# Kernel tuning notes

Measured on AMD Instinct MI355X. Metric: run time of the kernel, lower is better.

## Reference

```python
import jax, jax.numpy as jnp
import numpy as np

N, E, G = 50000, 800000, 64
IN, HID, T, EDGE_DIM, HLS = 32, 64, 2, 2, 32
# deg histogram: all nodes degree 16 -> avg_deg['log'] = log(16+1)
AVG_LOG = float(np.log(17.0))


def _pna(x, src, dst, eattr, We, be, Wpre, bpre, Wpost, bpost, Wlin, blin):
    """PNAConv with aggregators [mean,min,max,std], scalers [identity,amp,att],
    towers=T, pre_layers=1, post_layers=1, divide_input=False."""
    n, F = x.shape
    enc = eattr @ We + be                                   # [E, F] edge encoder
    # message: concat(x_i, x_j, edge) -> per-tower Linear(3F -> F)
    h = jnp.concatenate([x[dst], x[src], enc], axis=-1)     # [E, 3F] (same for all towers)
    m = jnp.einsum('ef,tfo->eto', h, Wpre) + bpre           # [E, T, F]
    ones = jnp.ones((m.shape[0],), m.dtype)
    cnt = jax.ops.segment_sum(ones, dst, num_segments=n)    # in-degree [N]
    d = jnp.maximum(cnt, 1.0)[:, None, None]
    s = jax.ops.segment_sum(m, dst, num_segments=n)
    mean = s / d
    msq = jax.ops.segment_sum(m * m, dst, num_segments=n) / d
    std = jnp.sqrt(jax.nn.relu(msq - mean * mean) + 1e-5)
    has = (cnt > 0)[:, None, None]
    mn = jnp.where(has, jax.ops.segment_min(m, dst, num_segments=n), 0.0)
    mx = jnp.where(has, jax.ops.segment_max(m, dst, num_segments=n), 0.0)
    agg = jnp.concatenate([mean, mn, mx, std], axis=-1)     # [N, T, 4F]
    logd = jnp.log(d + 1.0)
    scaled = jnp.concatenate([agg, agg * (logd / AVG_LOG), agg * (AVG_LOG / logd)], axis=-1)  # [N,T,12F]
    xt = jnp.broadcast_to(x[:, None, :], (n, Wpre.shape[0], F))
    out = jnp.concatenate([xt, scaled], axis=-1)            # [N, T, 13F]
    o = jnp.einsum('nti,tio->nto', out, Wpost) + bpost      # [N, T, F_out]
    return o.reshape(n, -1) @ Wlin + blin                   # [N, HID]


def setup_inputs():
    key = jax.random.key(0)
    ks = iter(jax.random.split(key, 48))
    def p(shape):
        return jax.random.normal(next(ks), shape, jnp.float32) * 0.05
    inp = {}
    inp['x'] = jax.random.normal(next(ks), (N, IN), jnp.float32)
    inp['edge_attr'] = jax.random.normal(next(ks), (E, EDGE_DIM), jnp.float32)
    inp['hls_attr'] = jax.random.normal(next(ks), (G, HLS), jnp.float32)
    inp['edge_index'] = jax.random.randint(next(ks), (2, E), 0, N)
    inp['batch'] = jnp.sort(jax.random.randint(next(ks), (N,), 0, G))
    Fo = HID // T
    for l, Fin in enumerate([IN, HID]):
        inp[f'We{l}'] = p((EDGE_DIM, Fin)); inp[f'be{l}'] = jnp.zeros((Fin,), jnp.float32)
        inp[f'Wpre{l}'] = p((T, 3 * Fin, Fin)); inp[f'bpre{l}'] = jnp.zeros((T, Fin), jnp.float32)
        inp[f'Wpost{l}'] = p((T, 13 * Fin, Fo)); inp[f'bpost{l}'] = jnp.zeros((T, Fo), jnp.float32)
        inp[f'Wlin{l}'] = p((HID, HID)); inp[f'blin{l}'] = jnp.zeros((HID,), jnp.float32)
    inp['W1'] = p((HID + HLS, 64)); inp['b1'] = jnp.zeros((64,), jnp.float32)
    inp['W2'] = p((64, 64)); inp['b2'] = jnp.zeros((64,), jnp.float32)
    inp['W3'] = p((64, 1)); inp['b3'] = jnp.zeros((1,), jnp.float32)
    return inp


def reference(x, edge_attr, hls_attr,
              We0, be0, Wpre0, bpre0, Wpost0, bpost0, Wlin0, blin0,
              We1, be1, Wpre1, bpre1, Wpost1, bpost1, Wlin1, blin1,
              W1, b1, W2, b2, W3, b3,
              edge_index, batch):
    src, dst = edge_index[0], edge_index[1]
    h = jax.nn.relu(_pna(x, src, dst, edge_attr, We0, be0, Wpre0, bpre0, Wpost0, bpost0, Wlin0, blin0))
    h = jax.nn.relu(_pna(h, src, dst, edge_attr, We1, be1, Wpre1, bpre1, Wpost1, bpost1, Wlin1, blin1))
    g = jax.ops.segment_sum(h, batch, num_segments=G)       # global_add_pool [G, HID]
    g = jnp.concatenate([g, hls_attr], axis=-1)
    g = jax.nn.relu(g @ W1 + b1)
    g = jax.nn.relu(g @ W2 + b2)
    return g @ W3 + b3                                      # [G, 1]
```

## Files before the change

### kernel.cpp

```cpp
#include <hip/hip_runtime.h>
#include <math.h>
#include <float.h>

#define NN 50000
#define EE 800000
#define CAP 64

typedef unsigned short ushort_t;
typedef short short8 __attribute__((ext_vector_type(8)));
typedef float floatx4 __attribute__((ext_vector_type(4)));

__device__ __constant__ float kAVG_LOG = 2.8332133440562162f;

__device__ inline ushort_t f2bf(float v) {
    union { float f; unsigned u; } x; x.f = v;
    unsigned r = x.u + 0x7fffu + ((x.u >> 16) & 1u);
    return (ushort_t)(r >> 16);
}
__device__ inline float bf2f(ushort_t b) {
    union { unsigned u; float f; } x; x.u = ((unsigned)b) << 16; return x.f;
}
__device__ inline float bitsf(unsigned u) {
    union { unsigned u; float f; } x; x.u = u; return x.f;
}
__device__ inline void splitbf(float v, ushort_t& hi, ushort_t& lo) {
    hi = f2bf(v);
    lo = f2bf(v - bf2f(hi));
}

__global__ __launch_bounds__(256) void init_kernel(int* cnt, float* pool, const float* __restrict__ x,
                                                   ushort_t* __restrict__ xb) {
    int i = blockIdx.x * 256 + threadIdx.x;
    if (i < NN * 32) xb[i] = f2bf(x[i]);
    if (i < NN) cnt[i] = 0;
    if (i < 64 * 64) pool[i] = 0.f;
}

__global__ __launch_bounds__(256) void build_csr(const int* __restrict__ ei, const float* __restrict__ ea,
                                                 int* __restrict__ cnt, uint2* __restrict__ csr) {
    int e = blockIdx.x * 256 + threadIdx.x;
    if (e >= EE) return;
    int s = ei[e];
    int d = ei[EE + e];
    float2 v = *(const float2*)(ea + 2 * e);
    int p = atomicAdd(&cnt[d], 1);
    if (p < CAP) {
        uint2 w;
        w.x = (unsigned)s;
        w.y = ((unsigned)f2bf(v.y) << 16) | (unsigned)f2bf(v.x);
        csr[d * CAP + p] = w;
    }
}

template <int F>
__device__ void prep_ab_dev(const float* __restrict__ We, const float* __restrict__ be,
                            const float* __restrict__ Wpre, const float* __restrict__ bpre,
                            float* __restrict__ U, float* __restrict__ Wab,
                            float* __restrict__ bias_ab) {
    const int TF = 2 * F;
    int tid = threadIdx.x;
    for (int idx = tid; idx < 2 * TF; idx += 256) {
        int c = idx / TF, f = idx % TF;
        int t = f / F, o = f % F;
        float s = 0.f;
        for (int g = 0; g < F; ++g)
            s += We[c * F + g] * Wpre[((size_t)t * 3 * F + 2 * F + g) * F + o];
        U[idx] = s;
    }
    for (int idx = tid; idx < F * 2 * TF; idx += 256) {
        int g = idx / (2 * TF), cc = idx % (2 * TF);
        int t, o, row;
        if (cc < TF) { t = cc / F; o = cc % F; row = g; }
        else { int c2 = cc - TF; t = c2 / F; o = c2 % F; row = F + g; }
        Wab[idx] = Wpre[((size_t)t * 3 * F + row) * F + o];
    }
    for (int cc = tid; cc < 2 * TF; cc += 256) {
        float v = 0.f;
        if (cc < TF) {
            int t = cc / F, o = cc % F;
            float s = 0.f;
            for (int g = 0; g < F; ++g)
                s += be[g] * Wpre[((size_t)t * 3 * F + 2 * F + g) * F + o];
            v = s + bpre[t * F + o];
        }
        bias_ab[cc] = v;
    }
}

template <int F>
__device__ void prep_zf_elem(int idx, const float* __restrict__ Wpost, const float* __restrict__ Wlin,
                             ushort_t* __restrict__ Bh, ushort_t* __restrict__ Bl) {
    const int KT = 9 * F;
    int jg = idx / KT, k = idx - jg * KT;
    int b = jg >> 6, j = jg & 63;
    float v = 0.f;
    if (k < F) {
        if (b == 0) {
#pragma unroll
            for (int t = 0; t < 2; ++t)
#pragma unroll
                for (int c = 0; c < 32; ++c)
                    v += Wpost[((size_t)t * 13 * F + k) * 32 + c] * Wlin[(t * 32 + c) * 64 + j];
        }
    } else {
        int r = k - F;
        int t = r / (4 * F), rr = r - t * 4 * F;
#pragma unroll
        for (int c = 0; c < 32; ++c)
            v += Wpost[((size_t)t * 13 * F + F + b * 4 * F + rr) * 32 + c] * Wlin[(t * 32 + c) * 64 + j];
    }
    ushort_t h_, l_;
    splitbf(v, h_, l_);
    Bh[(size_t)jg * KT + k] = h_;
    Bl[(size_t)jg * KT + k] = l_;
}

#define NZ0 216
#define NZ1 432

__global__ __launch_bounds__(256) void prep_all(
    const float* We0, const float* be0, const float* Wpre0, const float* bpre0,
    const float* Wpost0, const float* Wlin0, const float* bpost0, const float* blin0,
    const float* We1, const float* be1, const float* Wpre1, const float* bpre1,
    const float* Wpost1, const float* Wlin1, const float* bpost1, const float* blin1,
    float* U0, float* Wab0, float* bias_ab0, ushort_t* Bh0, ushort_t* Bl0, float* bias_zf0,
    float* U1, float* Wab1, float* bias_ab1, ushort_t* Bh1, ushort_t* Bl1, float* bias_zf1) {
    int b = blockIdx.x;
    int tid = threadIdx.x;
    if (b < NZ0) {
        prep_zf_elem<32>(b * 256 + tid, Wpost0, Wlin0, Bh0, Bl0);
    } else if (b < NZ0 + NZ1) {
        prep_zf_elem<64>((b - NZ0) * 256 + tid, Wpost1, Wlin1, Bh1, Bl1);
    } else if (b == NZ0 + NZ1) {
        prep_ab_dev<32>(We0, be0, Wpre0, bpre0, U0, Wab0, bias_ab0);
    } else if (b == NZ0 + NZ1 + 1) {
        prep_ab_dev<64>(We1, be1, Wpre1, bpre1, U1, Wab1, bias_ab1);
    } else {
        for (int j = tid; j < 64; j += 256) {
            float s0 = blin0[j], s1 = blin1[j];
#pragma unroll
            for (int t = 0; t < 2; ++t)
#pragma unroll
                for (int c = 0; c < 32; ++c) {
                    s0 += bpost0[t * 32 + c] * Wlin0[(t * 32 + c) * 64 + j];
                    s1 += bpost1[t * 32 + c] * Wlin1[(t * 32 + c) * 64 + j];
                }
            bias_zf0[j] = s0;
            bias_zf1[j] = s1;
        }
    }
}

__global__ __launch_bounds__(256) void gemm_bias(const float* __restrict__ A, const float* __restrict__ B,
                                                 const float* __restrict__ bias, float* __restrict__ Ca,
                                                 ushort_t* __restrict__ Cb, int M, int K, int Ncols, int bstart) {
    __shared__ float As[32][132];
    __shared__ float Bs[32][68];
    int m0 = blockIdx.x * 128, c0 = blockIdx.y * 64;
    int tid = threadIdx.x;
    int tx = tid & 15, ty = tid >> 4;
    int ms = tid >> 3, u = tid & 7;
    float acc[8][4] = {};
    for (int k0 = 0; k0 < K; k0 += 32) {
#pragma unroll
        for (int p = 0; p < 4; ++p) {
            int m = ms + 32 * p;
            int gm = m0 + m;
            float4 v = make_float4(0.f, 0.f, 0.f, 0.f);
            if (gm < M) v = *(const float4*)(A + (size_t)gm * K + k0 + u * 4);
            As[u * 4 + 0][m] = v.x; As[u * 4 + 1][m] = v.y;
            As[u * 4 + 2][m] = v.z; As[u * 4 + 3][m] = v.w;
        }
#pragma unroll
        for (int p = 0; p < 2; ++p) {
            int idx = tid + 256 * p;
            int kk = idx >> 4, q = idx & 15;
            *(float4*)&Bs[kk][q * 4] = *(const float4*)(B + (size_t)(k0 + kk) * Ncols + c0 + q * 4);
        }
        __syncthreads();
#pragma unroll 8
        for (int k = 0; k < 32; ++k) {
            float a0[8], b0[4];
            *(float4*)&a0[0] = *(const float4*)&As[k][ty * 8];
            *(float4*)&a0[4] = *(const float4*)&As[k][ty * 8 + 4];
            *(float4*)&b0[0] = *(const float4*)&Bs[k][tx * 4];
#pragma unroll
            for (int i = 0; i < 8; ++i)
#pragma unroll
                for (int j = 0; j < 4; ++j) acc[i][j] = fmaf(a0[i], b0[j], acc[i][j]);
        }
        __syncthreads();
    }
    float bj[4];
#pragma unroll
    for (int j = 0; j < 4; ++j) bj[j] = bias[c0 + tx * 4 + j];
    bool bside = (c0 >= bstart);
    int TFw = bstart;
#pragma unroll
    for (int i = 0; i < 8; ++i) {
        int gm = m0 + ty * 8 + i;
        if (gm >= M) continue;
        float v0 = acc[i][0] + bj[0], v1 = acc[i][1] + bj[1];
        float v2 = acc[i][2] + bj[2], v3 = acc[i][3] + bj[3];
        if (!bside) {
            *(float4*)(Ca + (size_t)gm * TFw + c0 + tx * 4) = make_float4(v0, v1, v2, v3);
        } else {
            ushort4 w;
            w.x = f2bf(v0); w.y = f2bf(v1); w.z = f2bf(v2); w.w = f2bf(v3);
            *(ushort4*)(Cb + (size_t)gm * TFw + (c0 - bstart) + tx * 4) = w;
        }
    }
}

template <int F>
__global__ __launch_bounds__(256) void aggregate(const float* __restrict__ ABa, const ushort_t* __restrict__ ABb,
                                                 const int* __restrict__ cnt, const uint2* __restrict__ csr,
                                                 const float* __restrict__ U,
                                                 ushort_t* __restrict__ agg_b, float2* __restrict__ sc) {
    const int TF = 2 * F;
    const int FPL = TF / 64;
    int lane = threadIdx.x & 63;
    int n = blockIdx.x * 4 + (threadIdx.x >> 6);
    if (n >= NN) return;
    int f0 = FPL * lane;

    float base[FPL], u0[FPL], u1[FPL], sum[FPL], sq[FPL], mn[FPL], mx[FPL];
#pragma unroll
    for (int r = 0; r < FPL; ++r) {
        base[r] = ABa[(size_t)n * TF + f0 + r];
        u0[r] = U[f0 + r];
        u1[r] = U[TF + f0 + r];
        sum[r] = 0.f; sq[r] = 0.f; mn[r] = FLT_MAX; mx[r] = -FLT_MAX;
    }
    int deg = cnt[n];
    int ec = deg < CAP ? deg : CAP;
    if (ec > 0) {
        int ebase = n * CAP;
        int myi = lane < ec ? lane : ec - 1;
        uint2 ent = csr[ebase + myi];
        int msrc = (int)ent.x;
        unsigned mea = ent.y;
        int e = 0;
        for (; e + 8 <= ec; e += 8) {
            int sb[8]; unsigned ep[8];
            unsigned wv[8];
#pragma unroll
            for (int i = 0; i < 8; ++i) {
                sb[i] = __shfl(msrc, e + i);
                ep[i] = (unsigned)__shfl((int)mea, e + i);
            }
#pragma unroll
            for (int i = 0; i < 8; ++i) {
                if constexpr (FPL == 2)
                    wv[i] = *(const unsigned*)(ABb + (size_t)sb[i] * TF + f0);
                else
                    wv[i] = ABb[(size_t)sb[i] * TF + f0];
            }
#pragma unroll
            for (int i = 0; i < 8; ++i) {
                float ex = bitsf(ep[i] << 16);
                float ey = bitsf(ep[i] & 0xffff0000u);
                float v[FPL];
                if constexpr (FPL == 2) {
                    v[0] = bitsf(wv[i] << 16);
                    v[1] = bitsf(wv[i] & 0xffff0000u);
                } else {
                    v[0] = bitsf(wv[i] << 16);
                }
#pragma unroll
                for (int r = 0; r < FPL; ++r) {
                    float q = fmaf(ex, u0[r], fmaf(ey, u1[r], v[r]));
                    sum[r] += q;
                    sq[r] = fmaf(q, q, sq[r]);
                    mn[r] = fminf(mn[r], q);
                    mx[r] = fmaxf(mx[r], q);
                }
            }
        }
        if (e < ec) {
            int sb[8]; unsigned ep[8];
            unsigned wv[8];
#pragma unroll
            for (int i = 0; i < 8; ++i) {
                sb[i] = __shfl(msrc, e + i);
                ep[i] = (unsigned)__shfl((int)mea, e + i);
            }
#pragma unroll
            for (int i = 0; i < 8; ++i) {
                if (e + i < ec) {
                    if constexpr (FPL == 2)
                        wv[i] = *(const unsigned*)(ABb + (size_t)sb[i] * TF + f0);
                    else
                        wv[i] = ABb[(size_t)sb[i] * TF + f0];
                }
            }
#pragma unroll
            for (int i = 0; i < 8; ++i) {
                if (e + i < ec) {
                    float ex = bitsf(ep[i] << 16);
                    float ey = bitsf(ep[i] & 0xffff0000u);
                    float v[FPL];
                    if constexpr (FPL == 2) {
                        v[0] = bitsf(wv[i] << 16);
                        v[1] = bitsf(wv[i] & 0xffff0000u);
                    } else {
                        v[0] = bitsf(wv[i] << 16);
                    }
#pragma unroll
                    for (int r = 0; r < FPL; ++r) {
                        float q = fmaf(ex, u0[r], fmaf(ey, u1[r], v[r]));
                        sum[r] += q;
                        sq[r] = fmaf(q, q, sq[r]);
                        mn[r] = fminf(mn[r], q);
                        mx[r] = fmaxf(mx[r], q);
                    }
                }
            }
        }
    }
    float d = (float)(deg > 1 ? deg : 1);
    float inv_d = 1.f / d;
    bool has = deg > 0;
#pragma unroll
    for (int r = 0; r < FPL; ++r) {
        float mean_q = sum[r] * inv_d;
        float var = sq[r] * inv_d - mean_q * mean_q;
        float stdv = sqrtf(fmaxf(var, 0.f) + 1e-5f);
        float mean = has ? base[r] + mean_q : 0.f;
        float vmn = has ? base[r] + mn[r] : 0.f;
        float vmx = has ? base[r] + mx[r] : 0.f;
        int f = f0 + r;
        int t = f / F, o = f - t * F;
        size_t rowb = (size_t)n * (4 * TF) + (size_t)t * (4 * F);
        agg_b[rowb + o] = f2bf(mean);
        agg_b[rowb + F + o] = f2bf(vmn);
        agg_b[rowb + 2 * F + o] = f2bf(vmx);
        agg_b[rowb + 3 * F + o] = f2bf(stdv);
    }
    if (lane == 0) {
        float logd = logf(d + 1.f);
        sc[n] = make_float2(logd / kAVG_LOG, kAVG_LOG / logd);
    }
}

template <int F, bool POOL>
__global__ __launch_bounds__(256, 2) void gemm_zf(
    const ushort_t* __restrict__ xs_b, const ushort_t* __restrict__ agg_b,
    const ushort_t* __restrict__ Bh, const ushort_t* __restrict__ Bl,
    const float* __restrict__ bias_zf, const float2* __restrict__ sc,
    float* __restrict__ H, ushort_t* __restrict__ H_b,
    const int* __restrict__ batch, float* __restrict__ pool) {
    const int KT = 9 * F;
    extern __shared__ char smem[];
    ushort_t* A_s  = (ushort_t*)smem;
    ushort_t* Bh_s = A_s + 128 * 40;
    ushort_t* Bl_s = Bh_s + 192 * 40;
    float* hbuf = (float*)smem;

    int m0 = blockIdx.x * 128;
    int tid = threadIdx.x;
    int lane = tid & 63;
    int wave = tid >> 6;
    int ln = lane & 15, quad = lane >> 4;

    floatx4 acc[8][3];
#pragma unroll
    for (int i = 0; i < 8; ++i)
#pragma unroll
        for (int j = 0; j < 3; ++j) acc[i][j] = (floatx4)(0.f);

    int arow = tid >> 2, asg = tid & 3;
    int bcol[3], bsg[3];
#pragma unroll
    for (int p = 0; p < 3; ++p) {
        int idx = tid + 256 * p;
        bcol[p] = idx >> 2;
        bsg[p] = idx & 3;
    }

    const short8 zero8 = {0, 0, 0, 0, 0, 0, 0, 0};
    short8 pa[2], pbh[3], pbl[3];
    {
        int c0 = asg * 8;
#pragma unroll
        for (int q = 0; q < 2; ++q) {
            int gm = m0 + arow + q * 64;
            pa[q] = zero8;
            if (gm < NN) pa[q] = *(const short8*)(xs_b + (size_t)gm * F + c0);
        }
#pragma unroll
        for (int p = 0; p < 3; ++p) {
            pbh[p] = *(const short8*)(Bh + (size_t)bcol[p] * KT + bsg[p] * 8);
            pbl[p] = *(const short8*)(Bl + (size_t)bcol[p] * KT + bsg[p] * 8);
        }
    }

    for (int k0 = 0; k0 < KT; k0 += 32) {
#pragma unroll
        for (int q = 0; q < 2; ++q)
            *(short8*)&A_s[(arow + q * 64) * 40 + asg * 8] = pa[q];
#pragma unroll
        for (int p = 0; p < 3; ++p) {
            *(short8*)&Bh_s[bcol[p] * 40 + bsg[p] * 8] = pbh[p];
            *(short8*)&Bl_s[bcol[p] * 40 + bsg[p] * 8] = pbl[p];
        }
        __syncthreads();
        short8 bh[3], bl[3];
#pragma unroll
        for (int b = 0; b < 3; ++b) {
            int col = b * 64 + wave * 16 + ln;
            bh[b] = *(short8*)&Bh_s[col * 40 + quad * 8];
            bl[b] = *(short8*)&Bl_s[col * 40 + quad * 8];
        }
        int kn = k0 + 32;
        if (kn < KT) {
            int c0 = kn + asg * 8;
#pragma unroll
            for (int q = 0; q < 2; ++q) {
                int gm = m0 + arow + q * 64;
                pa[q] = zero8;
                if (gm < NN) {
                    pa[q] = (c0 < F) ? *(const short8*)(xs_b + (size_t)gm * F + c0)
                                     : *(const short8*)(agg_b + (size_t)gm * 8 * F + (c0 - F));
                }
            }
#pragma unroll
            for (int p = 0; p < 3; ++p) {
                pbh[p] = *(const short8*)(Bh + (size_t)bcol[p] * KT + kn + bsg[p] * 8);
                pbl[p] = *(const short8*)(Bl + (size_t)bcol[p] * KT + kn + bsg[p] * 8);
            }
        }
#pragma unroll
        for (int rf = 0; rf < 8; ++rf) {
            short8 ah = *(short8*)&A_s[(rf * 16 + ln) * 40 + quad * 8];
#pragma unroll
            for (int b = 0; b < 3; ++b) {
                acc[rf][b] = __builtin_amdgcn_mfma_f32_16x16x32_bf16(ah, bh[b], acc[rf][b], 0, 0, 0);
                acc[rf][b] = __builtin_amdgcn_mfma_f32_16x16x32_bf16(ah, bl[b], acc[rf][b], 0, 0, 0);
            }
        }
        __syncthreads();
    }

    int ocol = wave * 16 + ln;
    float bcolv = bias_zf[ocol];

    if (POOL) __syncthreads();

#pragma unroll
    for (int rf = 0; rf < 8; ++rf) {
#pragma unroll
        for (int reg = 0; reg < 4; ++reg) {
            int r = rf * 16 + quad * 4 + reg;
            int gm = m0 + r;
            float2 s = make_float2(0.f, 0.f);
            if (gm < NN) s = sc[gm];
            float y = acc[rf][0][reg] + s.x * acc[rf][1][reg] + s.y * acc[rf][2][reg] + bcolv;
            y = fmaxf(y, 0.f);
            if (POOL) {
                hbuf[r * 68 + ocol] = (gm < NN) ? y : 0.f;
            } else if (gm < NN) {
                H[(size_t)gm * 64 + ocol] = y;
                H_b[(size_t)gm * 64 + ocol] = f2bf(y);
            }
        }
    }
    if (POOL) {
        __syncthreads();
        int col = tid & 63, grp = tid >> 6;
        float a = 0.f;
        int cur = -1;
        for (int i = 0; i < 32; ++i) {
            int r = grp * 32 + i;
            int gm = m0 + r;
            if (gm >= NN) break;
            int b = batch[gm];
            if (b != cur) {
                if (cur >= 0) atomicAdd(&pool[cur * 64 + col], a);
                cur = b; a = 0.f;
            }
            a += hbuf[r * 68 + col];
        }
        if (cur >= 0) atomicAdd(&pool[cur * 64 + col], a);
    }
}

__global__ __launch_bounds__(256) void head_kernel(const float* __restrict__ gpool, const float* __restrict__ hls,
                                                   const float* __restrict__ W1, const float* __restrict__ b1,
                                                   const float* __restrict__ W2, const float* __restrict__ b2,
                                                   const float* __restrict__ W3, const float* __restrict__ b3,
                                                   float* __restrict__ out) {
    __shared__ float gin[64][96];
    __shared__ float r1[64][64];
    __shared__ float r2[64][64];
    int tid = threadIdx.x;
    for (int idx = tid; idx < 64 * 96; idx += 256) {
        int g = idx / 96, j = idx % 96;
        gin[g][j] = (j < 64) ? gpool[g * 64 + j] : hls[g * 32 + (j - 64)];
    }
    __syncthreads();
    for (int idx = tid; idx < 64 * 64; idx += 256) {
        int g = idx / 64, j = idx % 64;
        float acc = b1[j];
        for (int k = 0; k < 96; ++k) acc = fmaf(gin[g][k], W1[k * 64 + j], acc);
        r1[g][j] = fmaxf(acc, 0.f);
    }
    __syncthreads();
    for (int idx = tid; idx < 64 * 64; idx += 256) {
        int g = idx / 64, j = idx % 64;
        float acc = b2[j];
        for (int k = 0; k < 64; ++k) acc = fmaf(r1[g][k], W2[k * 64 + j], acc);
        r2[g][j] = fmaxf(acc, 0.f);
    }
    __syncthreads();
    if (tid < 64) {
        float acc = b3[0];
        for (int k = 0; k < 64; ++k) acc = fmaf(r2[tid][k], W3[k], acc);
        out[tid] = acc;
    }
}

extern "C" void kernel_launch(void* const* d_in, const int* in_sizes, int n_in,
                              void* d_out, int out_size, void* d_ws, size_t ws_size,
                              hipStream_t stream) {
    (void)in_sizes; (void)n_in; (void)out_size; (void)ws_size;
    const float* x     = (const float*)d_in[0];
    const float* eattr = (const float*)d_in[1];
    const float* hls   = (const float*)d_in[2];
    const int*   eidx  = (const int*)d_in[3];
    const int*   batch = (const int*)d_in[4];
    const float* We[2]    = {(const float*)d_in[5],  (const float*)d_in[13]};
    const float* be[2]    = {(const float*)d_in[6],  (const float*)d_in[14]};
    const float* Wpre[2]  = {(const float*)d_in[7],  (const float*)d_in[15]};
    const float* bpre[2]  = {(const float*)d_in[8],  (const float*)d_in[16]};
    const float* Wpost[2] = {(const float*)d_in[9],  (const float*)d_in[17]};
    const float* bpost[2] = {(const float*)d_in[10], (const float*)d_in[18]};
    const float* Wlin[2]  = {(const float*)d_in[11], (const float*)d_in[19]};
    const float* blin[2]  = {(const float*)d_in[12], (const float*)d_in[20]};
    const float* W1 = (const float*)d_in[21]; const float* b1 = (const float*)d_in[22];
    const float* W2 = (const float*)d_in[23]; const float* b2 = (const float*)d_in[24];
    const float* W3 = (const float*)d_in[25]; const float* b3 = (const float*)d_in[26];
    float* out = (float*)d_out;

    char* ws = (char*)d_ws;
    size_t off = 0;
    auto carve = [&](size_t bytes) -> char* {
        char* p = ws + off;
        off = (off + bytes + 255) & ~(size_t)255;
        return p;
    };
    int*      cnt      = (int*)carve((size_t)NN * 4);
    uint2*    csr      = (uint2*)carve((size_t)NN * CAP * 8);
    float*    ABa      = (float*)carve((size_t)NN * 128 * 4);
    ushort_t* ABb      = (ushort_t*)carve((size_t)NN * 128 * 2);
    ushort_t* agg_b    = (ushort_t*)carve((size_t)NN * 512 * 2);
    float2*   sc       = (float2*)carve((size_t)NN * 8);
    ushort_t* xs_b     = (ushort_t*)carve((size_t)NN * 32 * 2);
    float*    h1       = (float*)carve((size_t)NN * 64 * 4);
    ushort_t* h1_b     = (ushort_t*)carve((size_t)NN * 64 * 2);
    float*    U0       = (float*)carve(256 * 4);
    float*    U1       = (float*)carve(256 * 4);
    float*    Wab0     = (float*)carve(16384 * 4);
    float*    Wab1     = (float*)carve(16384 * 4);
    float*    bias_ab0 = (float*)carve(256 * 4);
    float*    bias_ab1 = (float*)carve(256 * 4);
    ushort_t* Bh0      = (ushort_t*)carve((size_t)192 * 288 * 2);
    ushort_t* Bl0      = (ushort_t*)carve((size_t)192 * 288 * 2);
    ushort_t* Bh1      = (ushort_t*)carve((size_t)192 * 576 * 2);
    ushort_t* Bl1      = (ushort_t*)carve((size_t)192 * 576 * 2);
    float*    bias_zf0 = (float*)carve(64 * 4);
    float*    bias_zf1 = (float*)carve(64 * 4);
    float*    pool     = (float*)carve(64 * 64 * 4);

    const int MB128 = (NN + 127) / 128;
    const int SMEM_ZF = (128 * 40 + 192 * 40 + 192 * 40) * 2;

    init_kernel<<<(NN * 32 + 255) / 256, 256, 0, stream>>>(cnt, pool, x, xs_b);
    build_csr<<<(EE + 255) / 256, 256, 0, stream>>>(eidx, eattr, cnt, csr);
    prep_all<<<NZ0 + NZ1 + 3, 256, 0, stream>>>(
        We[0], be[0], Wpre[0], bpre[0], Wpost[0], Wlin[0], bpost[0], blin[0],
        We[1], be[1], Wpre[1], bpre[1], Wpost[1], Wlin[1], bpost[1], blin[1],
        U0, Wab0, bias_ab0, Bh0, Bl0, bias_zf0,
        U1, Wab1, bias_ab1, Bh1, Bl1, bias_zf1);

    gemm_bias<<<dim3(MB128, 2), 256, 0, stream>>>(x, Wab0, bias_ab0, ABa, ABb, NN, 32, 128, 64);
    aggregate<32><<<(NN + 3) / 4, 256, 0, stream>>>(ABa, ABb, cnt, csr, U0, agg_b, sc);
    gemm_zf<32, false><<<MB128, 256, SMEM_ZF, stream>>>(xs_b, agg_b, Bh0, Bl0, bias_zf0, sc,
                                                        h1, h1_b, batch, pool);

    gemm_bias<<<dim3(MB128, 4), 256, 0, stream>>>(h1, Wab1, bias_ab1, ABa, ABb, NN, 64, 256, 128);
    aggregate<64><<<(NN + 3) / 4, 256, 0, stream>>>(ABa, ABb, cnt, csr, U1, agg_b, sc);
    gemm_zf<64, true><<<MB128, 256, SMEM_ZF, stream>>>(h1_b, agg_b, Bh1, Bl1, bias_zf1, sc,
                                                       nullptr, nullptr, batch, pool);

    head_kernel<<<1, 256, 0, stream>>>(pool, hls, W1, b1, W2, b2, W3, b3, out);
}
```

Before: 375.7 us.

## Fuse init into prep kernel, co-schedule CSR build with first GEMM, pad counters

Three separate launches are folded into fewer. Initialization (bf16 conversion of x, zeroing counters and the pool) now runs as extra blocks of the weight-prep kernel. The CSR build and the first layer's bias GEMM are merged into one launch, with every fifth block doing a GEMM tile, so the memory-bound scatter and the compute GEMM overlap and launch gaps shrink. The per-node degree counters are padded to a 64-byte stride to cut atomic contention on shared cache lines. The cost is a larger counter array to zero and strided counter reads in the aggregate kernel.

```diff
diff --git a/kernel.cpp b/kernel.cpp
--- a/kernel.cpp
+++ b/kernel.cpp
@@ -5,6 +5,7 @@
 #define NN 50000
 #define EE 800000
 #define CAP 64
+#define CPAD 16
 
 typedef unsigned short ushort_t;
 typedef short short8 __attribute__((ext_vector_type(8)));
@@ -26,30 +27,6 @@
 __device__ inline void splitbf(float v, ushort_t& hi, ushort_t& lo) {
     hi = f2bf(v);
     lo = f2bf(v - bf2f(hi));
-}
-
-__global__ __launch_bounds__(256) void init_kernel(int* cnt, float* pool, const float* __restrict__ x,
-                                                   ushort_t* __restrict__ xb) {
-    int i = blockIdx.x * 256 + threadIdx.x;
-    if (i < NN * 32) xb[i] = f2bf(x[i]);
-    if (i < NN) cnt[i] = 0;
-    if (i < 64 * 64) pool[i] = 0.f;
-}
-
-__global__ __launch_bounds__(256) void build_csr(const int* __restrict__ ei, const float* __restrict__ ea,
-                                                 int* __restrict__ cnt, uint2* __restrict__ csr) {
-    int e = blockIdx.x * 256 + threadIdx.x;
-    if (e >= EE) return;
-    int s = ei[e];
-    int d = ei[EE + e];
-    float2 v = *(const float2*)(ea + 2 * e);
-    int p = atomicAdd(&cnt[d], 1);
-    if (p < CAP) {
-        uint2 w;
-        w.x = (unsigned)s;
-        w.y = ((unsigned)f2bf(v.y) << 16) | (unsigned)f2bf(v.x);
-        csr[d * CAP + p] = w;
-    }
 }
 
 template <int F>
@@ -117,16 +94,26 @@
 
 #define NZ0 216
 #define NZ1 432
-
-__global__ __launch_bounds__(256) void prep_all(
+#define PREPB (NZ0 + NZ1 + 3)
+#define INITB 6250
+
+__global__ __launch_bounds__(256) void prep_init(
     const float* We0, const float* be0, const float* Wpre0, const float* bpre0,
     const float* Wpost0, const float* Wlin0, const float* bpost0, const float* blin0,
     const float* We1, const float* be1, const float* Wpre1, const float* bpre1,
     const float* Wpost1, const float* Wlin1, const float* bpost1, const float* blin1,
     float* U0, float* Wab0, float* bias_ab0, ushort_t* Bh0, ushort_t* Bl0, float* bias_zf0,
-    float* U1, float* Wab1, float* bias_ab1, ushort_t* Bh1, ushort_t* Bl1, float* bias_zf1) {
+    float* U1, float* Wab1, float* bias_ab1, ushort_t* Bh1, ushort_t* Bl1, float* bias_zf1,
+    int* cnt, float* pool, const float* __restrict__ x, ushort_t* __restrict__ xb) {
     int b = blockIdx.x;
     int tid = threadIdx.x;
+    if (b >= PREPB) {
+        int i = (b - PREPB) * 256 + tid;
+        if (i < NN * 32) xb[i] = f2bf(x[i]);
+        if (i < NN * CPAD) cnt[i] = 0;
+        if (i < 64 * 64) pool[i] = 0.f;
+        return;
+    }
     if (b < NZ0) {
         prep_zf_elem<32>(b * 256 + tid, Wpost0, Wlin0, Bh0, Bl0);
     } else if (b < NZ0 + NZ1) {
@@ -151,12 +138,13 @@
     }
 }
 
-__global__ __launch_bounds__(256) void gemm_bias(const float* __restrict__ A, const float* __restrict__ B,
-                                                 const float* __restrict__ bias, float* __restrict__ Ca,
-                                                 ushort_t* __restrict__ Cb, int M, int K, int Ncols, int bstart) {
+__device__ void gemm_bias_block(const float* __restrict__ A, const float* __restrict__ B,
+                                const float* __restrict__ bias, float* __restrict__ Ca,
+                                ushort_t* __restrict__ Cb, int M, int K, int Ncols, int bstart,
+                                int mb, int cb) {
     __shared__ float As[32][132];
     __shared__ float Bs[32][68];
-    int m0 = blockIdx.x * 128, c0 = blockIdx.y * 64;
+    int m0 = mb * 128, c0 = cb * 64;
     int tid = threadIdx.x;
     int tx = tid & 15, ty = tid >> 4;
     int ms = tid >> 3, u = tid & 7;
@@ -212,6 +200,38 @@
     }
 }
 
+__global__ __launch_bounds__(256) void gemm_bias(const float* __restrict__ A, const float* __restrict__ B,
+                                                 const float* __restrict__ bias, float* __restrict__ Ca,
+                                                 ushort_t* __restrict__ Cb, int M, int K, int Ncols, int bstart) {
+    gemm_bias_block(A, B, bias, Ca, Cb, M, K, Ncols, bstart, blockIdx.x, blockIdx.y);
+}
+
+__global__ __launch_bounds__(256) void csr_gemm0(
+    const int* __restrict__ ei, const float* __restrict__ ea,
+    int* __restrict__ cnt, uint2* __restrict__ csr,
+    const float* __restrict__ A, const float* __restrict__ B, const float* __restrict__ bias,
+    float* __restrict__ Ca, ushort_t* __restrict__ Cb) {
+    int bx = blockIdx.x;
+    if (bx % 5 == 0) {
+        int g = bx / 5;
+        gemm_bias_block(A, B, bias, Ca, Cb, NN, 32, 128, 64, g % 391, g / 391);
+    } else {
+        int ce = bx - 1 - bx / 5;
+        int e = ce * 256 + threadIdx.x;
+        if (e >= EE) return;
+        int s = ei[e];
+        int d = ei[EE + e];
+        float2 v = *(const float2*)(ea + 2 * e);
+        int p = atomicAdd(&cnt[d * CPAD], 1);
+        if (p < CAP) {
+            uint2 w;
+            w.x = (unsigned)s;
+            w.y = ((unsigned)f2bf(v.y) << 16) | (unsigned)f2bf(v.x);
+            csr[d * CAP + p] = w;
+        }
+    }
+}
+
 template <int F>
 __global__ __launch_bounds__(256) void aggregate(const float* __restrict__ ABa, const ushort_t* __restrict__ ABb,
                                                  const int* __restrict__ cnt, const uint2* __restrict__ csr,
@@ -232,7 +252,7 @@
         u1[r] = U[TF + f0 + r];
         sum[r] = 0.f; sq[r] = 0.f; mn[r] = FLT_MAX; mx[r] = -FLT_MAX;
     }
-    int deg = cnt[n];
+    int deg = cnt[n * CPAD];
     int ec = deg < CAP ? deg : CAP;
     if (ec > 0) {
         int ebase = n * CAP;
@@ -549,7 +569,7 @@
         off = (off + bytes + 255) & ~(size_t)255;
         return p;
     };
-    int*      cnt      = (int*)carve((size_t)NN * 4);
+    int*      cnt      = (int*)carve((size_t)NN * CPAD * 4);
     uint2*    csr      = (uint2*)carve((size_t)NN * CAP * 8);
     float*    ABa      = (float*)carve((size_t)NN * 128 * 4);
     ushort_t* ABb      = (ushort_t*)carve((size_t)NN * 128 * 2);
@@ -574,16 +594,17 @@
 
     const int MB128 = (NN + 127) / 128;
     const int SMEM_ZF = (128 * 40 + 192 * 40 + 192 * 40) * 2;
-
-    init_kernel<<<(NN * 32 + 255) / 256, 256, 0, stream>>>(cnt, pool, x, xs_b);
-    build_csr<<<(EE + 255) / 256, 256, 0, stream>>>(eidx, eattr, cnt, csr);
-    prep_all<<<NZ0 + NZ1 + 3, 256, 0, stream>>>(
+    const int CSRB = (EE + 255) / 256;
+    const int FUSEDB = CSRB + MB128 * 2;
+
+    prep_init<<<PREPB + INITB, 256, 0, stream>>>(
         We[0], be[0], Wpre[0], bpre[0], Wpost[0], Wlin[0], bpost[0], blin[0],
         We[1], be[1], Wpre[1], bpre[1], Wpost[1], Wlin[1], bpost[1], blin[1],
         U0, Wab0, bias_ab0, Bh0, Bl0, bias_zf0,
-        U1, Wab1, bias_ab1, Bh1, Bl1, bias_zf1);
-
-    gemm_bias<<<dim3(MB128, 2), 256, 0, stream>>>(x, Wab0, bias_ab0, ABa, ABb, NN, 32, 128, 64);
+        U1, Wab1, bias_ab1, Bh1, Bl1, bias_zf1,
+        cnt, pool, x, xs_b);
+
+    csr_gemm0<<<FUSEDB, 256, 0, stream>>>(eidx, eattr, cnt, csr, x, Wab0, bias_ab0, ABa, ABb);
     aggregate<32><<<(NN + 3) / 4, 256, 0, stream>>>(ABa, ABb, cnt, csr, U0, agg_b, sc);
     gemm_zf<32, false><<<MB128, 256, SMEM_ZF, stream>>>(xs_b, agg_b, Bh0, Bl0, bias_zf0, sc,
                                                         h1, h1_b, batch, pool);
```

Measured after the change: 355.6 us. -5.3%, faster.
